# Kernel optimization log

Hardware: AMD Instinct MI355X
Metric: run time of the kernel (lower is better)

The kernel has to match this reference:

```python
import jax, jax.numpy as jnp
import numpy as np

WINDOW = 5  # pairs (i, j) with j in [i+1, i+5]
NEG = -1e30


def setup_inputs() -> dict:
    key = jax.random.key(0)
    k1, k2, k3, k4 = jax.random.split(key, 4)
    b, l, h = 32, 4096, 768
    words = jax.random.normal(k1, (b, l, h), dtype=jnp.float32)
    diff = jax.random.normal(k2, (b, l), dtype=jnp.float32)  # unused by module
    W = jax.random.normal(k3, (1, 2 * h), dtype=jnp.float32) * (1.0 / np.sqrt(2 * h))
    bias = jax.random.normal(k4, (1,), dtype=jnp.float32) * 0.01
    return {"words": words, "diff": diff, "W": W, "b": bias}


def reference(words, diff, W, b):
    # Original: for each (i, j) with 1 <= j-i <= 5, score = relu(Linear(cat(w_i, w_j)))
    # then max over all pairs -> (batch, 1).
    # Linear factorizes: cat(w_i, w_j) @ W.T = w_i @ w1 + w_j @ w2.
    h = words.shape[-1]
    w1, w2 = W[0, :h], W[0, h:]
    s = jnp.einsum('blh,h->bl', words, w1)  # contribution of left word i
    t = jnp.einsum('blh,h->bl', words, w2)  # contribution of right word j
    # shifted right-contributions for offsets 1..5; pad with NEG so relu -> 0
    # (valid since all real scores are >= 0 after relu and L >= 2)
    shifted = jnp.stack(
        [jnp.pad(t[:, k:], ((0, 0), (0, k)), constant_values=NEG) for k in range(1, WINDOW + 1)],
        axis=-1,
    )  # (b, l, 5)
    scores = jax.nn.relu(s[:, :, None] + shifted + b[0])  # (b, l, 5)
    out = jnp.max(scores.reshape(scores.shape[0], -1), axis=1, keepdims=True)  # (b, 1)
    return out
```

## Files before the change

### kernel.cpp

```cpp
#include <hip/hip_runtime.h>

#define BATCH 32
#define LSEQ  4096
#define HDIM  768
#define NEGV  (-1e30f)

__global__ __launch_bounds__(256) void st_kernel(const float* __restrict__ words,
                                                 const float* __restrict__ W,
                                                 float* __restrict__ s_buf,
                                                 float* __restrict__ t_buf,
                                                 int total_rows) {
    const int lane = threadIdx.x & 63;
    const int wave = threadIdx.x >> 6;
    const int wave_global = blockIdx.x * 4 + wave;
    const int total_waves = gridDim.x * 4;

    const float4* Wv = (const float4*)W;
    const float4 a0 = Wv[lane];
    const float4 a1 = Wv[lane + 64];
    const float4 a2 = Wv[lane + 128];
    const float4 b0 = Wv[192 + lane];
    const float4 b1 = Wv[192 + lane + 64];
    const float4 b2 = Wv[192 + lane + 128];

    for (int row = wave_global; row < total_rows; row += total_waves) {
        const float4* wp = (const float4*)words + (size_t)row * (HDIM / 4);
        const float4 x0 = wp[lane];
        const float4 x1 = wp[lane + 64];
        const float4 x2 = wp[lane + 128];

        float s = 0.f, t = 0.f;
        s += x0.x * a0.x; s += x0.y * a0.y; s += x0.z * a0.z; s += x0.w * a0.w;
        s += x1.x * a1.x; s += x1.y * a1.y; s += x1.z * a1.z; s += x1.w * a1.w;
        s += x2.x * a2.x; s += x2.y * a2.y; s += x2.z * a2.z; s += x2.w * a2.w;
        t += x0.x * b0.x; t += x0.y * b0.y; t += x0.z * b0.z; t += x0.w * b0.w;
        t += x1.x * b1.x; t += x1.y * b1.y; t += x1.z * b1.z; t += x1.w * b1.w;
        t += x2.x * b2.x; t += x2.y * b2.y; t += x2.z * b2.z; t += x2.w * b2.w;

        #pragma unroll
        for (int off = 32; off > 0; off >>= 1) {
            s += __shfl_down(s, off, 64);
            t += __shfl_down(t, off, 64);
        }
        if (lane == 0) {
            s_buf[row] = s;
            t_buf[row] = t;
        }
    }
}

__global__ __launch_bounds__(256) void max_kernel(const float* __restrict__ s_buf,
                                                  const float* __restrict__ t_buf,
                                                  const float* __restrict__ bias,
                                                  float* __restrict__ out) {
    const int b = blockIdx.x;
    const float* s = s_buf + (size_t)b * LSEQ;
    const float* t = t_buf + (size_t)b * LSEQ;

    float m = NEGV;
    for (int l = threadIdx.x; l < LSEQ; l += 256) {
        float tm = NEGV;
        #pragma unroll
        for (int k = 1; k <= 5; ++k) {
            if (l + k < LSEQ) tm = fmaxf(tm, t[l + k]);
        }
        m = fmaxf(m, s[l] + tm);
    }
    #pragma unroll
    for (int off = 32; off > 0; off >>= 1) {
        m = fmaxf(m, __shfl_down(m, off, 64));
    }
    __shared__ float red[4];
    if ((threadIdx.x & 63) == 0) red[threadIdx.x >> 6] = m;
    __syncthreads();
    if (threadIdx.x == 0) {
        float M = fmaxf(fmaxf(red[0], red[1]), fmaxf(red[2], red[3]));
        out[b] = fmaxf(0.f, M + bias[0]);
    }
}

extern "C" void kernel_launch(void* const* d_in, const int* in_sizes, int n_in,
                              void* d_out, int out_size, void* d_ws, size_t ws_size,
                              hipStream_t stream) {
    const float* words = (const float*)d_in[0];
    const float* W    = (const float*)d_in[2];
    const float* bias = (const float*)d_in[3];
    float* out = (float*)d_out;

    float* s_buf = (float*)d_ws;
    float* t_buf = s_buf + BATCH * LSEQ;

    const int total_rows = BATCH * LSEQ;
    st_kernel<<<4096, 256, 0, stream>>>(words, W, s_buf, t_buf, total_rows);
    max_kernel<<<BATCH, 256, 0, stream>>>(s_buf, t_buf, bias, out);
}
```

Before: 540.1 us.

## Process four rows per wave with 16-lane dot products and widen max kernel

Restructures the projection kernel so each wave handles four rows at once, with 16 lanes per row looping over 12 float4 chunks, which cuts the cross-lane shuffle reduction from 6 to 4 steps. The weight vectors are held in 96 registers per lane, and the grid is halved. The max kernel moves to 1024 threads per block so the per-batch reduction runs with more parallelism. The workload is bandwidth-bound at about 400MB of input, so the gains are likely small, and the extra register pressure may lower occupancy.

```diff
diff --git a/kernel.cpp b/kernel.cpp
--- a/kernel.cpp
+++ b/kernel.cpp
@@ -9,56 +9,53 @@
                                                  const float* __restrict__ W,
                                                  float* __restrict__ s_buf,
                                                  float* __restrict__ t_buf,
-                                                 int total_rows) {
+                                                 int total_groups) {
     const int lane = threadIdx.x & 63;
-    const int wave = threadIdx.x >> 6;
-    const int wave_global = blockIdx.x * 4 + wave;
+    const int sub  = lane & 15;
+    const int r    = lane >> 4;
+    const int wave_global = blockIdx.x * 4 + (threadIdx.x >> 6);
     const int total_waves = gridDim.x * 4;
 
     const float4* Wv = (const float4*)W;
-    const float4 a0 = Wv[lane];
-    const float4 a1 = Wv[lane + 64];
-    const float4 a2 = Wv[lane + 128];
-    const float4 b0 = Wv[192 + lane];
-    const float4 b1 = Wv[192 + lane + 64];
-    const float4 b2 = Wv[192 + lane + 128];
+    float4 a[12], b[12];
+    #pragma unroll
+    for (int j = 0; j < 12; ++j) {
+        a[j] = Wv[sub + 16 * j];
+        b[j] = Wv[192 + sub + 16 * j];
+    }
 
-    for (int row = wave_global; row < total_rows; row += total_waves) {
+    for (int g = wave_global; g < total_groups; g += total_waves) {
+        const int row = g * 4 + r;
         const float4* wp = (const float4*)words + (size_t)row * (HDIM / 4);
-        const float4 x0 = wp[lane];
-        const float4 x1 = wp[lane + 64];
-        const float4 x2 = wp[lane + 128];
-
         float s = 0.f, t = 0.f;
-        s += x0.x * a0.x; s += x0.y * a0.y; s += x0.z * a0.z; s += x0.w * a0.w;
-        s += x1.x * a1.x; s += x1.y * a1.y; s += x1.z * a1.z; s += x1.w * a1.w;
-        s += x2.x * a2.x; s += x2.y * a2.y; s += x2.z * a2.z; s += x2.w * a2.w;
-        t += x0.x * b0.x; t += x0.y * b0.y; t += x0.z * b0.z; t += x0.w * b0.w;
-        t += x1.x * b1.x; t += x1.y * b1.y; t += x1.z * b1.z; t += x1.w * b1.w;
-        t += x2.x * b2.x; t += x2.y * b2.y; t += x2.z * b2.z; t += x2.w * b2.w;
-
         #pragma unroll
-        for (int off = 32; off > 0; off >>= 1) {
-            s += __shfl_down(s, off, 64);
-            t += __shfl_down(t, off, 64);
+        for (int j = 0; j < 12; ++j) {
+            const float4 x = wp[sub + 16 * j];
+            s += x.x * a[j].x; s += x.y * a[j].y; s += x.z * a[j].z; s += x.w * a[j].w;
+            t += x.x * b[j].x; t += x.y * b[j].y; t += x.z * b[j].z; t += x.w * b[j].w;
         }
-        if (lane == 0) {
+        #pragma unroll
+        for (int off = 8; off > 0; off >>= 1) {
+            s += __shfl_down(s, off, 16);
+            t += __shfl_down(t, off, 16);
+        }
+        if (sub == 0) {
             s_buf[row] = s;
             t_buf[row] = t;
         }
     }
 }
 
-__global__ __launch_bounds__(256) void max_kernel(const float* __restrict__ s_buf,
-                                                  const float* __restrict__ t_buf,
-                                                  const float* __restrict__ bias,
-                                                  float* __restrict__ out) {
+__global__ __launch_bounds__(1024) void max_kernel(const float* __restrict__ s_buf,
+                                                   const float* __restrict__ t_buf,
+                                                   const float* __restrict__ bias,
+                                                   float* __restrict__ out) {
     const int b = blockIdx.x;
     const float* s = s_buf + (size_t)b * LSEQ;
     const float* t = t_buf + (size_t)b * LSEQ;
 
     float m = NEGV;
-    for (int l = threadIdx.x; l < LSEQ; l += 256) {
+    for (int l = threadIdx.x; l < LSEQ; l += 1024) {
         float tm = NEGV;
         #pragma unroll
         for (int k = 1; k <= 5; ++k) {
@@ -70,11 +67,13 @@
     for (int off = 32; off > 0; off >>= 1) {
         m = fmaxf(m, __shfl_down(m, off, 64));
     }
-    __shared__ float red[4];
+    __shared__ float red[16];
     if ((threadIdx.x & 63) == 0) red[threadIdx.x >> 6] = m;
     __syncthreads();
     if (threadIdx.x == 0) {
-        float M = fmaxf(fmaxf(red[0], red[1]), fmaxf(red[2], red[3]));
+        float M = NEGV;
+        #pragma unroll
+        for (int i = 0; i < 16; ++i) M = fmaxf(M, red[i]);
         out[b] = fmaxf(0.f, M + bias[0]);
     }
 }
@@ -90,7 +89,7 @@
     float* s_buf = (float*)d_ws;
     float* t_buf = s_buf + BATCH * LSEQ;
 
-    const int total_rows = BATCH * LSEQ;
-    st_kernel<<<4096, 256, 0, stream>>>(words, W, s_buf, t_buf, total_rows);
-    max_kernel<<<BATCH, 256, 0, stream>>>(s_buf, t_buf, bias, out);
+    const int total_groups = (BATCH * LSEQ) / 4;
+    st_kernel<<<2048, 256, 0, stream>>>(words, W, s_buf, t_buf, total_groups);
+    max_kernel<<<BATCH, 1024, 0, stream>>>(s_buf, t_buf, bias, out);
 }
```

Result: faster. 528.0 us (-2.2%).
